# Kernel optimization log

Hardware: AMD Instinct MI355X
Metric: run time of the kernel (lower is better)

Reference implementation:

```python
import jax, jax.numpy as jnp
import numpy as np

# dims
T, B, D = 128, 512, 512          # seq, batch, d_input = dim_aug_state*n_agent
M, H, DH, DFF = 6, 2, 32, 64     # mem_len, heads, d_head_inner, d_ff_inner
ACT = 64                          # dim_action*n_agent
BG = 0.1                          # GRU-gate bias (GTrXL)


def _ln(t, g, b):
    mu = t.mean(-1, keepdims=True)
    var = ((t - mu) ** 2).mean(-1, keepdims=True)
    return (t - mu) / jnp.sqrt(var + 1e-5) * g + b


def _rel_shift(x):
    # x: [T, J, B, H] -> TransformerXL relative shift
    Tq, J = x.shape[0], x.shape[1]
    zp = jnp.zeros((Tq, 1) + x.shape[2:], x.dtype)
    x = jnp.concatenate([zp, x], axis=1)              # [T, J+1, B, H]
    x = x.reshape((J + 1, Tq) + x.shape[2:])[1:]      # [J, T, B, H]
    return x.reshape((Tq, J) + x.shape[2:])


def _gate(x, y, W, b):
    # GRU-style gating g(x, y): x = residual stream, y = new branch output
    lin = lambda t, i: t @ W[i] + b[i]
    r = jax.nn.sigmoid(lin(y, 0) + lin(x, 1))
    z = jax.nn.sigmoid(lin(y, 2) + lin(x, 3) - BG)
    h = jnp.tanh(lin(y, 4) + (r * x) @ W[5] + b[5])
    return (1.0 - z) * x + z * h


def setup_inputs() -> dict:
    key = jax.random.key(0)
    ks = iter(jax.random.split(key, 32))
    rn = lambda shape, s=0.02: jax.random.normal(next(ks), shape, jnp.float32) * s
    return dict(
        aug_states=jax.random.normal(next(ks), (T, B, D), jnp.float32),
        action=jax.random.normal(next(ks), (B, ACT), jnp.float32),
        memory=jnp.zeros((M, B, D), jnp.float32),
        W_q=rn((D, H * DH)), W_kv=rn((D, 2 * H * DH)), W_p=rn((D, H * DH)), W_out=rn((H * DH, D)),
        u=rn((H, DH)), v=rn((H, DH)),
        ln1_g=jnp.ones(D), ln1_b=jnp.zeros(D), ln2_g=jnp.ones(D), ln2_b=jnp.zeros(D),
        ff_W1=rn((D, DFF)), ff_b1=jnp.zeros(DFF), ff_W2=rn((DFF, D)), ff_b2=jnp.zeros(D),
        g1_W=rn((6, D, D)), g1_b=jnp.zeros((6, D)), g2_W=rn((6, D, D)), g2_b=jnp.zeros((6, D)),
        d1_W=rn((D, 1024)), d1_b=jnp.zeros(1024),
        d2_W=rn((1024 + ACT, 512)), d2_b=jnp.zeros(512),
        d3_W=rn((512, 300)), d3_b=jnp.zeros(300),
        d4_W=rn((300, 1)), d4_b=jnp.zeros(1),
    )


def reference(aug_states, action, memory, W_q, W_kv, W_p, W_out, u, v,
              ln1_g, ln1_b, ln2_g, ln2_b, ff_W1, ff_b1, ff_W2, ff_b2,
              g1_W, g1_b, g2_W, g2_b, d1_W, d1_b, d2_W, d2_b, d3_W, d3_b, d4_W, d4_b):
    x = aug_states                                    # [T, B, D]
    J = T + M
    # sinusoidal relative position embeddings for positions J-1 .. 0
    pos = jnp.arange(J - 1, -1, -1.0, dtype=jnp.float32)
    inv_freq = 1.0 / (10000.0 ** (jnp.arange(0, D, 2, dtype=jnp.float32) / D))
    si = pos[:, None] * inv_freq[None, :]
    pos_emb = jnp.concatenate([jnp.sin(si), jnp.cos(si)], axis=-1)   # [J, D]

    # --- stable (pre-LN + gated) TransformerXL layer ---
    src2 = _ln(x, ln1_g, ln1_b)
    cat = jnp.concatenate([memory, src2], axis=0)     # [J, B, D]
    k, vv = jnp.split(cat @ W_kv, 2, axis=-1)
    q = (src2 @ W_q).reshape(T, B, H, DH)
    k = k.reshape(J, B, H, DH)
    vv = vv.reshape(J, B, H, DH)
    p = (pos_emb @ W_p).reshape(J, H, DH)
    content = jnp.einsum("ibhd,jbhd->ijbh", q + u, k)
    position = _rel_shift(jnp.einsum("ibhd,jhd->ijbh", q + v, p))
    attn = content + position                         # [T, J, B, H]
    mask = jnp.arange(J)[None, :] > (jnp.arange(T)[:, None] + M)     # causal w/ memory offset
    attn = jnp.where(mask[:, :, None, None], -jnp.inf, attn)
    attn = jax.nn.softmax(attn * (1.0 / np.sqrt(DH)), axis=1)
    av = jnp.einsum("ijbh,jbhd->ibhd", attn, vv).reshape(T, B, H * DH)
    src = _gate(x, av @ W_out, g1_W, g1_b)
    ff = jax.nn.relu(_ln(src, ln2_g, ln2_b) @ ff_W1 + ff_b1) @ ff_W2 + ff_b2
    out = _gate(src, ff, g2_W, g2_b)                  # [T, B, D]

    # --- mean pool + MLP critic head ---
    ts = out.mean(axis=0)                             # [B, D]
    h1 = jax.nn.relu(ts @ d1_W + d1_b)
    h = jnp.concatenate([h1, action], axis=1)
    h = jax.nn.relu(h @ d2_W + d2_b)
    h = jax.nn.relu(h @ d3_W + d3_b)
    return jax.nn.relu(h @ d4_W + d4_b)               # [B, 1]
```

## Files before the change

kernel.cpp:

```cpp
#include <hip/hip_runtime.h>
#include <math.h>

namespace {

constexpr int kT = 128, kB = 512, kD = 512, kM = 6, kH = 2;
constexpr int kJ = kT + kM;
constexpr float kBG = 0.1f;
constexpr int kTB = kT * kB;
constexpr int kBK = 32;

typedef __attribute__((ext_vector_type(8))) short bf16x8;
typedef __attribute__((ext_vector_type(4))) float f32x4;
typedef __attribute__((ext_vector_type(8))) unsigned short us8;
typedef __attribute__((ext_vector_type(4))) unsigned short us4;

__device__ __forceinline__ float sigmoidf_(float x) {
  return 1.0f / (1.0f + __expf(-x));
}

__device__ __forceinline__ unsigned short bf16u(float f) {
  union { float f; unsigned u; } c; c.f = f;
  unsigned r = c.u + 0x7fffu + ((c.u >> 16) & 1u);
  return (unsigned short)(r >> 16);
}

__device__ __forceinline__ float b2f(unsigned short u) {
  union { unsigned u; float f; } c; c.u = (unsigned)u << 16;
  return c.f;
}

__device__ __forceinline__ void gl_lds16(const void* g, void* l) {
  __builtin_amdgcn_global_load_lds(
      (const __attribute__((address_space(1))) unsigned int*)g,
      (__attribute__((address_space(3))) unsigned int*)l, 16, 0, 0);
}

template <int N>
__device__ __forceinline__ void wvm_() {
  asm volatile("s_waitcnt vmcnt(%0)" :: "n"(N) : "memory");
}
__device__ __forceinline__ void bar_() { __builtin_amdgcn_s_barrier(); }
__device__ __forceinline__ void cfence_() { asm volatile("" ::: "memory"); }

__global__ __launch_bounds__(256) void transp_kernel(const float* __restrict__ W,
                                                     unsigned short* __restrict__ Wt,
                                                     int K, int N) {
  __shared__ float t[32][33];
  const int n0 = blockIdx.x * 32, k0 = blockIdx.y * 32;
  const float* Wb = W + (size_t)blockIdx.z * K * N;
  unsigned short* Wtb = Wt + (size_t)blockIdx.z * K * N;
  int tx = threadIdx.x & 31, ty = threadIdx.x >> 5;
#pragma unroll
  for (int r = 0; r < 32; r += 8)
    t[ty + r][tx] = Wb[(size_t)(k0 + ty + r) * N + n0 + tx];
  __syncthreads();
#pragma unroll
  for (int r = 0; r < 32; r += 8)
    Wtb[(size_t)(n0 + ty + r) * K + k0 + tx] = bf16u(t[tx][ty + r]);
}

__global__ __launch_bounds__(256) void conv_bf16_kernel(const float* __restrict__ in,
                                                        unsigned short* __restrict__ outb,
                                                        size_t n) {
  size_t idx = ((size_t)blockIdx.x * 256 + threadIdx.x) * 8;
  if (idx >= n) return;
  float4 a = *(const float4*)(in + idx);
  float4 c = *(const float4*)(in + idx + 4);
  us8 o;
  o[0] = bf16u(a.x); o[1] = bf16u(a.y); o[2] = bf16u(a.z); o[3] = bf16u(a.w);
  o[4] = bf16u(c.x); o[5] = bf16u(c.y); o[6] = bf16u(c.z); o[7] = bf16u(c.w);
  *(us8*)(outb + idx) = o;
}

__global__ __launch_bounds__(256) void ln1_dual_kernel(const float* __restrict__ in,
                                                       const float* __restrict__ g,
                                                       const float* __restrict__ b,
                                                       unsigned short* __restrict__ outLN,
                                                       unsigned short* __restrict__ outRaw,
                                                       int nrows) {
  int wave = threadIdx.x >> 6, lane = threadIdx.x & 63;
  int row = blockIdx.x * 4 + wave;
  if (row >= nrows) return;
  const float* p = in + (size_t)row * kD + lane * 8;
  float4 a = *(const float4*)p;
  float4 c = *(const float4*)(p + 4);
  float v[8] = {a.x, a.y, a.z, a.w, c.x, c.y, c.z, c.w};
  float s = 0.f;
#pragma unroll
  for (int i = 0; i < 8; ++i) s += v[i];
#pragma unroll
  for (int off = 32; off; off >>= 1) s += __shfl_xor(s, off);
  float mu = s * (1.0f / 512.0f);
  float q = 0.f;
#pragma unroll
  for (int i = 0; i < 8; ++i) { float d = v[i] - mu; q += d * d; }
#pragma unroll
  for (int off = 32; off; off >>= 1) q += __shfl_xor(q, off);
  float rstd = rsqrtf(q * (1.0f / 512.0f) + 1e-5f);
  us8 oln, oraw;
#pragma unroll
  for (int i = 0; i < 8; ++i) {
    int col = lane * 8 + i;
    oln[i] = bf16u((v[i] - mu) * rstd * g[col] + b[col]);
    oraw[i] = bf16u(v[i]);
  }
  size_t off8 = (size_t)row * kD + lane * 8;
  *(us8*)(outLN + off8) = oln;
  *(us8*)(outRaw + off8) = oraw;
}

__global__ __launch_bounds__(256) void ln_b16_kernel(const unsigned short* __restrict__ in,
                                                     const float* __restrict__ g,
                                                     const float* __restrict__ b,
                                                     unsigned short* __restrict__ outb,
                                                     int nrows) {
  int wave = threadIdx.x >> 6, lane = threadIdx.x & 63;
  int row = blockIdx.x * 4 + wave;
  if (row >= nrows) return;
  us8 iv = *(const us8*)(in + (size_t)row * kD + lane * 8);
  float v[8];
#pragma unroll
  for (int i = 0; i < 8; ++i) v[i] = b2f(iv[i]);
  float s = 0.f;
#pragma unroll
  for (int i = 0; i < 8; ++i) s += v[i];
#pragma unroll
  for (int off = 32; off; off >>= 1) s += __shfl_xor(s, off);
  float mu = s * (1.0f / 512.0f);
  float q = 0.f;
#pragma unroll
  for (int i = 0; i < 8; ++i) { float d = v[i] - mu; q += d * d; }
#pragma unroll
  for (int off = 32; off; off >>= 1) q += __shfl_xor(q, off);
  float rstd = rsqrtf(q * (1.0f / 512.0f) + 1e-5f);
  us8 o;
#pragma unroll
  for (int i = 0; i < 8; ++i) {
    int col = lane * 8 + i;
    o[i] = bf16u((v[i] - mu) * rstd * g[col] + b[col]);
  }
  *(us8*)(outb + (size_t)row * kD + lane * 8) = o;
}

template <int TN, int EPI>
__global__ __launch_bounds__(256) void mfma_gemm_bt(
    const unsigned short* __restrict__ A, const unsigned short* __restrict__ Bt,
    int K, const float* __restrict__ bias, void* __restrict__ Cv, int N) {
  constexpr int MI = (TN == 128) ? 4 : 2;
  constexpr int NJ = 4;
  constexpr int BCH = TN * 64 / 1024;
  constexpr int NLD = 2 + BCH / 4;
  __shared__ __align__(16) unsigned short As[3][128 * kBK];
  __shared__ __align__(16) unsigned short Bs[3][TN * kBK];
  const int tid = threadIdx.x;
  const int lane = tid & 63, wv = tid >> 6;
  const int ml = lane & 15, qd = lane >> 4;
  const int m0 = blockIdx.y * 128, n0 = blockIdx.x * TN;
  const int mw0 = (TN == 128) ? (wv >> 1) * 64 : wv * 32;
  const int nw0 = (TN == 128) ? (wv & 1) * 64 : 0;
  const size_t ldA = (size_t)K * 2, ldB = (size_t)K * 2;
  const char* Ab = (const char*)A + (size_t)m0 * ldA;
  const char* Bb = (const char*)Bt + (size_t)n0 * ldB;
  auto stg = [&](int k0, int buf) {
#pragma unroll
    for (int c = wv; c < 8; c += 4) {
      int fb = c * 1024 + lane * 16;
      gl_lds16(Ab + (size_t)(fb >> 6) * ldA + (fb & 63) + (size_t)k0 * 2,
               (char*)As[buf] + fb);
    }
#pragma unroll
    for (int c = wv; c < BCH; c += 4) {
      int fb = c * 1024 + lane * 16;
      gl_lds16(Bb + (size_t)(fb >> 6) * ldB + (fb & 63) + (size_t)k0 * 2,
               (char*)Bs[buf] + fb);
    }
  };
  f32x4 acc[MI][NJ];
#pragma unroll
  for (int i = 0; i < MI; ++i)
#pragma unroll
    for (int j = 0; j < NJ; ++j) acc[i][j] = (f32x4)0.f;
  stg(0, 0);
  stg(kBK, 1);
  int cb = 0;
  for (int k0 = 0; k0 < K; k0 += kBK) {
    const int sb = (cb == 0) ? 2 : cb - 1;
    if (k0 + 2 * kBK < K) { stg(k0 + 2 * kBK, sb); wvm_<2 * NLD>(); }
    else if (k0 + kBK < K) { wvm_<NLD>(); }
    else { wvm_<0>(); }
    bar_(); cfence_();
    bf16x8 af[MI], bfr[NJ];
#pragma unroll
    for (int i = 0; i < MI; ++i)
      af[i] = *(const bf16x8*)(As[cb] + (mw0 + i * 16 + ml) * kBK + qd * 8);
#pragma unroll
    for (int j = 0; j < NJ; ++j)
      bfr[j] = *(const bf16x8*)(Bs[cb] + (nw0 + j * 16 + ml) * kBK + qd * 8);
    __builtin_amdgcn_s_setprio(1);
#pragma unroll
    for (int i = 0; i < MI; ++i)
#pragma unroll
      for (int j = 0; j < NJ; ++j)
        acc[i][j] = __builtin_amdgcn_mfma_f32_16x16x32_bf16(af[i], bfr[j], acc[i][j], 0, 0, 0);
    __builtin_amdgcn_s_setprio(0);
    cfence_(); bar_();
    cb = (cb == 2) ? 0 : cb + 1;
  }
#pragma unroll
  for (int i = 0; i < MI; ++i)
#pragma unroll
    for (int j = 0; j < NJ; ++j)
#pragma unroll
      for (int r = 0; r < 4; ++r) {
        int m = m0 + mw0 + i * 16 + qd * 4 + r;
        int n = n0 + nw0 + j * 16 + ml;
        float val = acc[i][j][r];
        if (EPI >= 2) val += bias[n];
        if (EPI == 2) val = fmaxf(val, 0.f);
        size_t idx = (size_t)m * N + n;
        if (EPI == 0) ((float*)Cv)[idx] = val;
        else ((unsigned short*)Cv)[idx] = bf16u(val);
      }
}

template <int NBLOG>
__device__ __forceinline__ void xcd_decode(int& m0, int& n0, int tileN) {
  const int L = blockIdx.x;
  const int xcd = L & 7;
  const int s = L >> 3;
  const int mgPerX = (int)(gridDim.x >> (3 + NBLOG));
  const int mg = xcd * mgPerX + (s >> NBLOG);
  const int nb = s & ((1 << NBLOG) - 1);
  m0 = mg * 128;
  n0 = nb * tileN;
}

__global__ __launch_bounds__(256) void mfma_gate_rz(
    const unsigned short* __restrict__ Yb, const unsigned short* __restrict__ Xb,
    const unsigned short* __restrict__ Wt, const float* __restrict__ gb,
    unsigned short* __restrict__ RX, unsigned short* __restrict__ Zq) {
  __shared__ __align__(16) unsigned short As[3][128 * kBK];
  __shared__ __align__(16) unsigned short Bs[3][128 * kBK];
  const int tid = threadIdx.x;
  const int lane = tid & 63, wv = tid >> 6;
  const int ml = lane & 15, qd = lane >> 4;
  int m0, n0;
  xcd_decode<3>(m0, n0, 128);
  const int nhalf = n0 >> 9;
  const int n0e = n0 & 511;
  const int mw0 = (wv >> 1) * 64, nw0 = (wv & 1) * 64;
  const size_t ld = (size_t)kD * 2;
  const size_t DD = (size_t)kD * kD;
  const char* Abp[2]; const char* Bbp[2];
  {
    const unsigned short* Ap[2] = {Yb, Xb};
#pragma unroll
    for (int p = 0; p < 2; ++p) {
      Abp[p] = (const char*)Ap[p] + (size_t)m0 * ld;
      Bbp[p] = (const char*)(Wt + (size_t)(2 * nhalf + p) * DD) + (size_t)n0e * ld;
    }
  }
  auto stg = [&](const char* Ab, const char* Bb, int k0, int buf) {
#pragma unroll
    for (int c = wv; c < 8; c += 4) {
      int fb = c * 1024 + lane * 16;
      size_t go = (size_t)(fb >> 6) * ld + (fb & 63) + (size_t)k0 * 2;
      gl_lds16(Ab + go, (char*)As[buf] + fb);
      gl_lds16(Bb + go, (char*)Bs[buf] + fb);
    }
  };
  f32x4 acc[4][4];
#pragma unroll
  for (int i = 0; i < 4; ++i)
#pragma unroll
    for (int j = 0; j < 4; ++j) acc[i][j] = (f32x4)0.f;
  stg(Abp[0], Bbp[0], 0, 0);
  stg(Abp[0], Bbp[0], kBK, 1);
  int cb = 0;
#pragma unroll
  for (int p = 0; p < 2; ++p) {
    for (int k = 0; k < 16; ++k) {
      const int sb = (cb == 0) ? 2 : cb - 1;
      if (k < 14) { stg(Abp[p], Bbp[p], (k + 2) * kBK, sb); wvm_<8>(); }
      else if (p < 1) { stg(Abp[p + 1], Bbp[p + 1], (k - 14) * kBK, sb); wvm_<8>(); }
      else if (k == 14) { wvm_<4>(); }
      else { wvm_<0>(); }
      bar_(); cfence_();
      bf16x8 af[4], bfr[4];
#pragma unroll
      for (int i = 0; i < 4; ++i)
        af[i] = *(const bf16x8*)(As[cb] + (mw0 + i * 16 + ml) * kBK + qd * 8);
#pragma unroll
      for (int j = 0; j < 4; ++j)
        bfr[j] = *(const bf16x8*)(Bs[cb] + (nw0 + j * 16 + ml) * kBK + qd * 8);
      __builtin_amdgcn_s_setprio(1);
#pragma unroll
      for (int i = 0; i < 4; ++i)
#pragma unroll
        for (int j = 0; j < 4; ++j)
          acc[i][j] = __builtin_amdgcn_mfma_f32_16x16x32_bf16(af[i], bfr[j], acc[i][j], 0, 0, 0);
      __builtin_amdgcn_s_setprio(0);
      cfence_(); bar_();
      cb = (cb == 2) ? 0 : cb + 1;
    }
  }
  if (nhalf == 0) {
#pragma unroll
    for (int i = 0; i < 4; ++i)
#pragma unroll
      for (int j = 0; j < 4; ++j)
#pragma unroll
        for (int r = 0; r < 4; ++r) {
          int m = m0 + mw0 + i * 16 + qd * 4 + r;
          int n = n0e + nw0 + j * 16 + ml;
          float rg = sigmoidf_(acc[i][j][r] + gb[n] + gb[kD + n]);
          size_t idx = (size_t)m * kD + n;
          RX[idx] = bf16u(rg * b2f(Xb[idx]));
        }
  } else {
#pragma unroll
    for (int i = 0; i < 4; ++i)
#pragma unroll
      for (int j = 0; j < 4; ++j)
#pragma unroll
        for (int r = 0; r < 4; ++r) {
          int m = m0 + mw0 + i * 16 + qd * 4 + r;
          int n = n0e + nw0 + j * 16 + ml;
          float z = sigmoidf_(acc[i][j][r] + gb[2 * kD + n] + gb[3 * kD + n] - kBG);
          Zq[(size_t)m * kD + n] = (unsigned short)(z * 65535.f + 0.5f);
        }
  }
}

template <bool POOL>
__global__ __launch_bounds__(256) void mfma_gate_h(
    const unsigned short* __restrict__ Yb, const unsigned short* __restrict__ RXb,
    const unsigned short* __restrict__ Xb, const unsigned short* __restrict__ Wt,
    const float* __restrict__ gb, const unsigned short* __restrict__ Zq,
    unsigned short* __restrict__ OUTb, float* __restrict__ TS, int rowoff) {
  __shared__ __align__(16) unsigned short As[3][128 * kBK];
  __shared__ __align__(16) unsigned short Bs[3][128 * kBK];
  const int tid = threadIdx.x;
  const int lane = tid & 63, wv = tid >> 6;
  const int ml = lane & 15, qd = lane >> 4;
  int m0, n0;
  xcd_decode<2>(m0, n0, 128);
  const int mw0 = (wv >> 1) * 64, nw0 = (wv & 1) * 64;
  const size_t ld = (size_t)kD * 2;
  const size_t DD = (size_t)kD * kD;
  const char* Abp[2]; const char* Bbp[2];
  {
    const unsigned short* Ap[2] = {Yb, RXb};
#pragma unroll
    for (int p = 0; p < 2; ++p) {
      Abp[p] = (const char*)Ap[p] + (size_t)m0 * ld;
      Bbp[p] = (const char*)(Wt + (size_t)(4 + p) * DD) + (size_t)n0 * ld;
    }
  }
  auto stg = [&](const char* Ab, const char* Bb, int k0, int buf) {
#pragma unroll
    for (int c = wv; c < 8; c += 4) {
      int fb = c * 1024 + lane * 16;
      size_t go = (size_t)(fb >> 6) * ld + (fb & 63) + (size_t)k0 * 2;
      gl_lds16(Ab + go, (char*)As[buf] + fb);
      gl_lds16(Bb + go, (char*)Bs[buf] + fb);
    }
  };
  f32x4 acc[4][4];
#pragma unroll
  for (int i = 0; i < 4; ++i)
#pragma unroll
    for (int j = 0; j < 4; ++j) acc[i][j] = (f32x4)0.f;
  stg(Abp[0], Bbp[0], 0, 0);
  stg(Abp[0], Bbp[0], kBK, 1);
  int cb = 0;
#pragma unroll
  for (int p = 0; p < 2; ++p) {
    for (int k = 0; k < 16; ++k) {
      const int sb = (cb == 0) ? 2 : cb - 1;
      if (k < 14) { stg(Abp[p], Bbp[p], (k + 2) * kBK, sb); wvm_<8>(); }
      else if (p < 1) { stg(Abp[p + 1], Bbp[p + 1], (k - 14) * kBK, sb); wvm_<8>(); }
      else if (k == 14) { wvm_<4>(); }
      else { wvm_<0>(); }
      bar_(); cfence_();
      bf16x8 af[4], bfr[4];
#pragma unroll
      for (int i = 0; i < 4; ++i)
        af[i] = *(const bf16x8*)(As[cb] + (mw0 + i * 16 + ml) * kBK + qd * 8);
#pragma unroll
      for (int j = 0; j < 4; ++j)
        bfr[j] = *(const bf16x8*)(Bs[cb] + (nw0 + j * 16 + ml) * kBK + qd * 8);
      __builtin_amdgcn_s_setprio(1);
#pragma unroll
      for (int i = 0; i < 4; ++i)
#pragma unroll
        for (int j = 0; j < 4; ++j)
          acc[i][j] = __builtin_amdgcn_mfma_f32_16x16x32_bf16(af[i], bfr[j], acc[i][j], 0, 0, 0);
      __builtin_amdgcn_s_setprio(0);
      cfence_(); bar_();
      cb = (cb == 2) ? 0 : cb + 1;
    }
  }
#pragma unroll
  for (int i = 0; i < 4; ++i)
#pragma unroll
    for (int j = 0; j < 4; ++j)
#pragma unroll
      for (int r = 0; r < 4; ++r) {
        int m = m0 + mw0 + i * 16 + qd * 4 + r;
        int n = n0 + nw0 + j * 16 + ml;
        size_t idx = (size_t)m * kD + n;
        float z = (float)Zq[idx] * (1.0f / 65535.0f);
        float hc = tanhf(acc[i][j][r] + gb[4 * kD + n] + gb[5 * kD + n]);
        float val = (1.0f - z) * b2f(Xb[idx]) + z * hc;
        if (POOL) {
          int b = (rowoff + m) & (kB - 1);
          atomicAdd(TS + (size_t)b * kD + n, val * (1.0f / kT));
        } else {
          OUTb[idx] = bf16u(val);
        }
      }
}

__global__ __launch_bounds__(64) void posp_kernel(const float* __restrict__ Wp,
                                                  float* __restrict__ P) {
  __shared__ float emb[512];
  int jj = blockIdx.x;
  int t = threadIdx.x;
  float pos = (float)(kJ - 1 - jj);
#pragma unroll
  for (int r = 0; r < 8; ++r) {
    int d = t + r * 64;
    int i = (d < 256) ? d : d - 256;
    float invf = expf(-((float)(2 * i) * (1.0f / 512.0f)) * 9.210340371976184f);
    float si = pos * invf;
    emb[d] = (d < 256) ? sinf(si) : cosf(si);
  }
  __syncthreads();
  float acc = 0.f;
  for (int d = 0; d < 512; ++d) acc = fmaf(emb[d], Wp[d * 64 + t], acc);
  P[jj * 64 + t] = acc;
}

__global__ __launch_bounds__(128) void attn_kernel(
    const float* __restrict__ Q, const unsigned short* __restrict__ KV,
    const float* __restrict__ P, const float* __restrict__ U,
    const float* __restrict__ V, unsigned short* __restrict__ AV) {
  __shared__ float ks[kJ][32];
  __shared__ float vs[kJ][32];
  __shared__ float ps[32][kJ + 2];
  const int b = blockIdx.x, h = blockIdx.y;
  const int tid = threadIdx.x;
  for (int idx = tid; idx < kJ * 8; idx += 128) {
    int j = idx >> 3, seg = idx & 7;
    const unsigned short* src = KV + ((size_t)(j * kB + b)) * 128 + h * 32 + seg * 4;
    us4 kq = *(const us4*)src;
    us4 vq = *(const us4*)(src + 64);
#pragma unroll
    for (int e = 0; e < 4; ++e) {
      ks[j][seg * 4 + e] = b2f(kq[e]);
      vs[j][seg * 4 + e] = b2f(vq[e]);
    }
  }
  for (int idx = tid; idx < kJ * 8; idx += 128) {
    int j = idx >> 3, seg = idx & 7;
    float4 pq = *(const float4*)(P + j * 64 + h * 32 + seg * 4);
    ps[seg * 4 + 0][j] = pq.x;
    ps[seg * 4 + 1][j] = pq.y;
    ps[seg * 4 + 2][j] = pq.z;
    ps[seg * 4 + 3][j] = pq.w;
  }
  __syncthreads();
  const int i = tid;
  float qu[32], qv[32];
  const float* qp = Q + ((size_t)(i * kB + b)) * 64 + h * 32;
#pragma unroll
  for (int d = 0; d < 32; ++d) {
    float qd = qp[d];
    qu[d] = qd + U[h * 32 + d];
    qv[d] = qd + V[h * 32 + d];
  }
  float m = -INFINITY, l = 0.f, acc[32] = {};
  const float scale = 0.17677669529663687f;
  for (int j = 0; j <= i + kM; ++j) {
    float s = 0.f;
#pragma unroll
    for (int d = 0; d < 32; d += 4) {
      float4 k4 = *(const float4*)&ks[j][d];
      s = fmaf(qu[d + 0], k4.x, s);
      s = fmaf(qu[d + 1], k4.y, s);
      s = fmaf(qu[d + 2], k4.z, s);
      s = fmaf(qu[d + 3], k4.w, s);
    }
    int jj = j + (kT - 1) - i;
#pragma unroll
    for (int d = 0; d < 32; ++d) s = fmaf(qv[d], ps[d][jj], s);
    float ls = s * scale;
    float nm = fmaxf(m, ls);
    float w = __expf(ls - nm);
    float f = __expf(m - nm);
    l = l * f + w;
#pragma unroll
    for (int d = 0; d < 32; d += 4) {
      float4 v4 = *(const float4*)&vs[j][d];
      acc[d + 0] = fmaf(acc[d + 0], f, w * v4.x);
      acc[d + 1] = fmaf(acc[d + 1], f, w * v4.y);
      acc[d + 2] = fmaf(acc[d + 2], f, w * v4.z);
      acc[d + 3] = fmaf(acc[d + 3], f, w * v4.w);
    }
    m = nm;
  }
  float inv = 1.0f / l;
  unsigned short* o = AV + ((size_t)(i * kB + b)) * 64 + h * 32;
#pragma unroll
  for (int d = 0; d < 32; ++d) o[d] = bf16u(acc[d] * inv);
}

template <int ACTF, bool DUAL>
__global__ __launch_bounds__(256) void gemm_kernel(
    const float* __restrict__ A1, const float* __restrict__ Bm1, int K1,
    const float* __restrict__ A2, const float* __restrict__ Bm2, int K2,
    const float* __restrict__ bias, float* __restrict__ C, int Mrows, int N) {
  __shared__ float As[16][68];
  __shared__ float Bs[16][68];
  const int tid = threadIdx.x;
  const int tx = tid & 15, ty = tid >> 4;
  const int m0 = blockIdx.y * 64, n0 = blockIdx.x * 64;
  const int ar = tid >> 2, aseg = tid & 3;
  float acc[4][4] = {};
#pragma unroll
  for (int pass = 0; pass < (DUAL ? 2 : 1); ++pass) {
    const float* A = (DUAL && pass) ? A2 : A1;
    const float* Bm = (DUAL && pass) ? Bm2 : Bm1;
    const int K = (DUAL && pass) ? K2 : K1;
    for (int k0 = 0; k0 < K; k0 += 16) {
      {
        int row = m0 + ar;
        int kb = k0 + aseg * 4;
        float x0 = 0.f, x1 = 0.f, x2 = 0.f, x3 = 0.f;
        if (row < Mrows) {
          const float* ap = A + (size_t)row * K + kb;
          if (kb + 3 < K) {
            float4 t = *(const float4*)ap;
            x0 = t.x; x1 = t.y; x2 = t.z; x3 = t.w;
          } else {
            if (kb + 0 < K) x0 = ap[0];
            if (kb + 1 < K) x1 = ap[1];
            if (kb + 2 < K) x2 = ap[2];
          }
        }
        As[aseg * 4 + 0][ar] = x0;
        As[aseg * 4 + 1][ar] = x1;
        As[aseg * 4 + 2][ar] = x2;
        As[aseg * 4 + 3][ar] = x3;
      }
      {
        int krow = k0 + ty;
        int nb = n0 + tx * 4;
        float y0 = 0.f, y1 = 0.f, y2 = 0.f, y3 = 0.f;
        if (krow < K) {
          const float* bp = Bm + (size_t)krow * N + nb;
          if (nb + 3 < N) {
            float4 t = *(const float4*)bp;
            y0 = t.x; y1 = t.y; y2 = t.z; y3 = t.w;
          } else {
            if (nb + 0 < N) y0 = bp[0];
            if (nb + 1 < N) y1 = bp[1];
            if (nb + 2 < N) y2 = bp[2];
          }
        }
        *(float4*)&Bs[ty][tx * 4] = make_float4(y0, y1, y2, y3);
      }
      __syncthreads();
#pragma unroll
      for (int kk = 0; kk < 16; ++kk) {
        float a[4], bb[4];
        *(float4*)a = *(const float4*)&As[kk][ty * 4];
        *(float4*)bb = *(const float4*)&Bs[kk][tx * 4];
#pragma unroll
        for (int i = 0; i < 4; ++i)
#pragma unroll
          for (int j = 0; j < 4; ++j) acc[i][j] = fmaf(a[i], bb[j], acc[i][j]);
      }
      __syncthreads();
    }
  }
#pragma unroll
  for (int i = 0; i < 4; ++i) {
    int m = m0 + ty * 4 + i;
    if (m >= Mrows) continue;
#pragma unroll
    for (int j = 0; j < 4; ++j) {
      int n = n0 + tx * 4 + j;
      if (n >= N) continue;
      float val = acc[i][j];
      if (bias) val += bias[n];
      if (ACTF == 1) val = fmaxf(val, 0.f);
      C[(size_t)m * N + n] = val;
    }
  }
}

}

extern "C" void kernel_launch(void* const* d_in, const int* in_sizes, int n_in,
                              void* d_out, int out_size, void* d_ws, size_t ws_size,
                              hipStream_t stream) {
  (void)in_sizes; (void)n_in; (void)out_size;
  const float* aug    = (const float*)d_in[0];
  const float* action = (const float*)d_in[1];
  const float* memory = (const float*)d_in[2];
  const float* W_q    = (const float*)d_in[3];
  const float* W_kv   = (const float*)d_in[4];
  const float* W_p    = (const float*)d_in[5];
  const float* W_out  = (const float*)d_in[6];
  const float* u      = (const float*)d_in[7];
  const float* v      = (const float*)d_in[8];
  const float* ln1_g  = (const float*)d_in[9];
  const float* ln1_b  = (const float*)d_in[10];
  const float* ln2_g  = (const float*)d_in[11];
  const float* ln2_b  = (const float*)d_in[12];
  const float* ff_W1  = (const float*)d_in[13];
  const float* ff_b1  = (const float*)d_in[14];
  const float* ff_W2  = (const float*)d_in[15];
  const float* ff_b2  = (const float*)d_in[16];
  const float* g1_W   = (const float*)d_in[17];
  const float* g1_b   = (const float*)d_in[18];
  const float* g2_W   = (const float*)d_in[19];
  const float* g2_b   = (const float*)d_in[20];
  const float* d1_W   = (const float*)d_in[21];
  const float* d1_b   = (const float*)d_in[22];
  const float* d2_W   = (const float*)d_in[23];
  const float* d2_b   = (const float*)d_in[24];
  const float* d3_W   = (const float*)d_in[25];
  const float* d3_b   = (const float*)d_in[26];
  const float* d4_W   = (const float*)d_in[27];
  const float* d4_b   = (const float*)d_in[28];
  float* out = (float*)d_out;

  char* base = (char*)d_ws;
  auto alloc = [&](size_t bytes) -> char* {
    char* p = base;
    base += (bytes + 255) & ~(size_t)255;
    return p;
  };
  unsigned short* Wqt  = (unsigned short*)alloc((size_t)64 * 512 * 2);
  unsigned short* Wkvt = (unsigned short*)alloc((size_t)128 * 512 * 2);
  unsigned short* Wot  = (unsigned short*)alloc((size_t)512 * 64 * 2);
  unsigned short* Wf1t = (unsigned short*)alloc((size_t)64 * 512 * 2);
  unsigned short* Wf2t = (unsigned short*)alloc((size_t)512 * 64 * 2);
  unsigned short* G1t  = (unsigned short*)alloc((size_t)6 * 512 * 512 * 2);
  unsigned short* G2t  = (unsigned short*)alloc((size_t)6 * 512 * 512 * 2);
  unsigned short* Memb = (unsigned short*)alloc((size_t)3072 * 512 * 2);
  unsigned short* KVb  = (unsigned short*)alloc((size_t)kJ * kB * 128 * 2);
  float* Qb  = (float*)alloc((size_t)kTB * 64 * 4);
  unsigned short* AVb = (unsigned short*)alloc((size_t)kTB * 64 * 2);
  unsigned short* Xb  = (unsigned short*)alloc((size_t)kTB * kD * 2);
  float* Pb  = (float*)alloc((size_t)kJ * 64 * 4);
  float* TSb = (float*)alloc((size_t)kB * kD * 4);
  float* H1b = (float*)alloc((size_t)kB * 1024 * 4);
  float* H2b = (float*)alloc((size_t)kB * 512 * 4);
  float* H3b = (float*)alloc((size_t)kB * 320 * 4);
  size_t fixedBytes = (size_t)(base - (char*)d_ws);
  const size_t ln1Bytes = (size_t)kTB * kD * 2;
  int nch = 1;
  while (nch < 32) {
    size_t chunkBytes = (size_t)(kTB / nch) * 4224 + 4096;
    size_t reuse = chunkBytes > ln1Bytes ? chunkBytes : ln1Bytes;
    if (fixedBytes + reuse <= ws_size) break;
    nch <<= 1;
  }
  const int CR = kTB / nch;
  char* R = base;
  unsigned short* L1b = (unsigned short*)R;
  char* rp = R;
  auto ralloc = [&](size_t bytes) -> char* {
    char* p = rp;
    rp += (bytes + 255) & ~(size_t)255;
    return p;
  };
  unsigned short* Ycb   = (unsigned short*)ralloc((size_t)CR * 512 * 2);
  unsigned short* RXcb  = (unsigned short*)ralloc((size_t)CR * 512 * 2);
  unsigned short* SRCcb = (unsigned short*)ralloc((size_t)CR * 512 * 2);
  unsigned short* LN2cb = (unsigned short*)ralloc((size_t)CR * 512 * 2);
  unsigned short* F1cb  = (unsigned short*)ralloc((size_t)CR * 64 * 2);
  unsigned short* Zqb = LN2cb;

  const float* np = nullptr;
  const int MG = CR / 128;

  hipMemsetAsync(TSb, 0, (size_t)kB * kD * sizeof(float), stream);
  transp_kernel<<<dim3(2, 16, 1), 256, 0, stream>>>(W_q, Wqt, 512, 64);
  transp_kernel<<<dim3(4, 16, 1), 256, 0, stream>>>(W_kv, Wkvt, 512, 128);
  transp_kernel<<<dim3(16, 2, 1), 256, 0, stream>>>(W_out, Wot, 64, 512);
  transp_kernel<<<dim3(2, 16, 1), 256, 0, stream>>>(ff_W1, Wf1t, 512, 64);
  transp_kernel<<<dim3(16, 2, 1), 256, 0, stream>>>(ff_W2, Wf2t, 64, 512);
  transp_kernel<<<dim3(16, 16, 6), 256, 0, stream>>>(g1_W, G1t, 512, 512);
  transp_kernel<<<dim3(16, 16, 6), 256, 0, stream>>>(g2_W, G2t, 512, 512);
  conv_bf16_kernel<<<(3072 * 512 / 8 + 255) / 256, 256, 0, stream>>>(
      memory, Memb, (size_t)3072 * 512);
  ln1_dual_kernel<<<kTB / 4, 256, 0, stream>>>(aug, ln1_g, ln1_b, L1b, Xb, kTB);
  mfma_gemm_bt<128, 1><<<dim3(1, 3072 / 128), 256, 0, stream>>>(
      Memb, Wkvt, 512, np, KVb, 128);
  mfma_gemm_bt<128, 1><<<dim3(1, kTB / 128), 256, 0, stream>>>(
      L1b, Wkvt, 512, np, KVb + (size_t)3072 * 128, 128);
  mfma_gemm_bt<64, 0><<<dim3(1, kTB / 128), 256, 0, stream>>>(
      L1b, Wqt, 512, np, Qb, 64);
  posp_kernel<<<kJ, 64, 0, stream>>>(W_p, Pb);
  attn_kernel<<<dim3(kB, kH), 128, 0, stream>>>(Qb, KVb, Pb, u, v, AVb);

  for (int c = 0; c < nch; ++c) {
    const int R0 = c * CR;
    const unsigned short* Xc = Xb + (size_t)R0 * kD;
    mfma_gemm_bt<128, 1><<<dim3(4, MG), 256, 0, stream>>>(
        AVb + (size_t)R0 * 64, Wot, 64, np, Ycb, 512);
    mfma_gate_rz<<<8 * MG, 256, 0, stream>>>(Ycb, Xc, G1t, g1_b, RXcb, Zqb);
    mfma_gate_h<false><<<4 * MG, 256, 0, stream>>>(
        Ycb, RXcb, Xc, G1t, g1_b, Zqb, SRCcb, nullptr, R0);
    ln_b16_kernel<<<CR / 4, 256, 0, stream>>>(SRCcb, ln2_g, ln2_b, LN2cb, CR);
    mfma_gemm_bt<64, 2><<<dim3(1, MG), 256, 0, stream>>>(
        LN2cb, Wf1t, 512, ff_b1, F1cb, 64);
    mfma_gemm_bt<128, 3><<<dim3(4, MG), 256, 0, stream>>>(
        F1cb, Wf2t, 64, ff_b2, Ycb, 512);
    mfma_gate_rz<<<8 * MG, 256, 0, stream>>>(Ycb, SRCcb, G2t, g2_b, RXcb, Zqb);
    mfma_gate_h<true><<<4 * MG, 256, 0, stream>>>(
        Ycb, RXcb, SRCcb, G2t, g2_b, Zqb, nullptr, TSb, R0);
  }

  gemm_kernel<1, false><<<dim3(16, kB / 64), 256, 0, stream>>>(
      TSb, d1_W, 512, np, np, 0, d1_b, H1b, kB, 1024);
  gemm_kernel<1, true><<<dim3(8, kB / 64), 256, 0, stream>>>(
      H1b, d2_W, 1024, action, d2_W + (size_t)1024 * 512, 64, d2_b, H2b, kB, 512);
  gemm_kernel<1, false><<<dim3(5, kB / 64), 256, 0, stream>>>(
      H2b, d3_W, 512, np, np, 0, d3_b, H3b, kB, 300);
  gemm_kernel<1, false><<<dim3(1, kB / 64), 256, 0, stream>>>(
      H3b, d4_W, 300, np, np, 0, d4_b, out, kB, 1);
}
```

Baseline: 1.547 ms.

## Drop persistent bf16 residual buffer, reconvert per chunk, chunk LN1 projections

The full-size bf16 copy of the input (Xb) is no longer written by the LN1 kernel. Each main-loop chunk now reconverts its slice of the fp32 input into a reused buffer, and gate_h writes its output in place over that buffer. The LN1/Q/KV projection is split into chunks over a smaller scratch area, and the main chunk count starts at 2 to fit the reduced workspace. The setprio hints around the MFMA loop are also removed. This saves a large global write and shrinks the working set for better cache locality, at the cost of re-reading the fp32 input and launching more kernels.

```diff
diff --git a/kernel.cpp b/kernel.cpp
--- a/kernel.cpp
+++ b/kernel.cpp
@@ -106,7 +106,7 @@
   }
   size_t off8 = (size_t)row * kD + lane * 8;
   *(us8*)(outLN + off8) = oln;
-  *(us8*)(outRaw + off8) = oraw;
+  if (outRaw) *(us8*)(outRaw + off8) = oraw;
 }
 
 __global__ __launch_bounds__(256) void ln_b16_kernel(const unsigned short* __restrict__ in,
@@ -196,13 +196,11 @@
 #pragma unroll
     for (int j = 0; j < NJ; ++j)
       bfr[j] = *(const bf16x8*)(Bs[cb] + (nw0 + j * 16 + ml) * kBK + qd * 8);
-    __builtin_amdgcn_s_setprio(1);
 #pragma unroll
     for (int i = 0; i < MI; ++i)
 #pragma unroll
       for (int j = 0; j < NJ; ++j)
         acc[i][j] = __builtin_amdgcn_mfma_f32_16x16x32_bf16(af[i], bfr[j], acc[i][j], 0, 0, 0);
-    __builtin_amdgcn_s_setprio(0);
     cfence_(); bar_();
     cb = (cb == 2) ? 0 : cb + 1;
   }
@@ -638,10 +636,12 @@
   const float* d4_b   = (const float*)d_in[28];
   float* out = (float*)d_out;
 
+  auto A256 = [](size_t b) { return (b + 255) & ~(size_t)255; };
+
   char* base = (char*)d_ws;
   auto alloc = [&](size_t bytes) -> char* {
     char* p = base;
-    base += (bytes + 255) & ~(size_t)255;
+    base += A256(bytes);
     return p;
   };
   unsigned short* Wqt  = (unsigned short*)alloc((size_t)64 * 512 * 2);
@@ -651,43 +651,48 @@
   unsigned short* Wf2t = (unsigned short*)alloc((size_t)512 * 64 * 2);
   unsigned short* G1t  = (unsigned short*)alloc((size_t)6 * 512 * 512 * 2);
   unsigned short* G2t  = (unsigned short*)alloc((size_t)6 * 512 * 512 * 2);
-  unsigned short* Memb = (unsigned short*)alloc((size_t)3072 * 512 * 2);
-  unsigned short* KVb  = (unsigned short*)alloc((size_t)kJ * kB * 128 * 2);
-  float* Qb  = (float*)alloc((size_t)kTB * 64 * 4);
-  unsigned short* AVb = (unsigned short*)alloc((size_t)kTB * 64 * 2);
-  unsigned short* Xb  = (unsigned short*)alloc((size_t)kTB * kD * 2);
+  unsigned short* AVb  = (unsigned short*)alloc((size_t)kTB * 64 * 2);
   float* Pb  = (float*)alloc((size_t)kJ * 64 * 4);
   float* TSb = (float*)alloc((size_t)kB * kD * 4);
   float* H1b = (float*)alloc((size_t)kB * 1024 * 4);
   float* H2b = (float*)alloc((size_t)kB * 512 * 4);
   float* H3b = (float*)alloc((size_t)kB * 320 * 4);
-  size_t fixedBytes = (size_t)(base - (char*)d_ws);
-  const size_t ln1Bytes = (size_t)kTB * kD * 2;
-  int nch = 1;
-  while (nch < 32) {
-    size_t chunkBytes = (size_t)(kTB / nch) * 4224 + 4096;
-    size_t reuse = chunkBytes > ln1Bytes ? chunkBytes : ln1Bytes;
-    if (fixedBytes + reuse <= ws_size) break;
+  const size_t persist = (size_t)(base - (char*)d_ws);
+
+  const size_t membB = A256((size_t)3072 * 512 * 2);
+  const size_t kvbB  = A256((size_t)kJ * kB * 128 * 2);
+  const size_t qbB   = A256((size_t)kTB * 64 * 4);
+  int nchp = 1;
+  while (nchp < 32) {
+    size_t l1B = A256((size_t)(kTB / nchp) * 512 * 2);
+    if (persist + membB + kvbB + qbB + l1B <= ws_size) break;
+    nchp <<= 1;
+  }
+  int nch = 2;
+  while (nch < 64) {
+    size_t CRi = (size_t)kTB / nch;
+    size_t mainB = 4 * A256(CRi * 512 * 2) + A256(CRi * 64 * 2);
+    if (persist + mainB <= ws_size) break;
     nch <<= 1;
   }
-  const int CR = kTB / nch;
-  char* R = base;
-  unsigned short* L1b = (unsigned short*)R;
-  char* rp = R;
-  auto ralloc = [&](size_t bytes) -> char* {
-    char* p = rp;
-    rp += (bytes + 255) & ~(size_t)255;
-    return p;
-  };
-  unsigned short* Ycb   = (unsigned short*)ralloc((size_t)CR * 512 * 2);
-  unsigned short* RXcb  = (unsigned short*)ralloc((size_t)CR * 512 * 2);
-  unsigned short* SRCcb = (unsigned short*)ralloc((size_t)CR * 512 * 2);
-  unsigned short* LN2cb = (unsigned short*)ralloc((size_t)CR * 512 * 2);
-  unsigned short* F1cb  = (unsigned short*)ralloc((size_t)CR * 64 * 2);
+  const int CRp = kTB / nchp;
+  const int CR  = kTB / nch;
+  const int MG  = CR / 128;
+
+  char* U = base;
+  unsigned short* Memb = (unsigned short*)U;
+  unsigned short* KVb  = (unsigned short*)(U + membB);
+  float*          Qb   = (float*)(U + membB + kvbB);
+  unsigned short* L1c  = (unsigned short*)(U + membB + kvbB + qbB);
+  const size_t rb = A256((size_t)CR * 512 * 2);
+  unsigned short* XSc   = (unsigned short*)U;
+  unsigned short* Ycb   = (unsigned short*)(U + rb);
+  unsigned short* RXcb  = (unsigned short*)(U + 2 * rb);
+  unsigned short* LN2cb = (unsigned short*)(U + 3 * rb);
+  unsigned short* F1cb  = (unsigned short*)(U + 4 * rb);
   unsigned short* Zqb = LN2cb;
 
   const float* np = nullptr;
-  const int MG = CR / 128;
 
   hipMemsetAsync(TSb, 0, (size_t)kB * kD * sizeof(float), stream);
   transp_kernel<<<dim3(2, 16, 1), 256, 0, stream>>>(W_q, Wqt, 512, 64);
@@ -697,34 +702,39 @@
   transp_kernel<<<dim3(16, 2, 1), 256, 0, stream>>>(ff_W2, Wf2t, 64, 512);
   transp_kernel<<<dim3(16, 16, 6), 256, 0, stream>>>(g1_W, G1t, 512, 512);
   transp_kernel<<<dim3(16, 16, 6), 256, 0, stream>>>(g2_W, G2t, 512, 512);
+  posp_kernel<<<kJ, 64, 0, stream>>>(W_p, Pb);
   conv_bf16_kernel<<<(3072 * 512 / 8 + 255) / 256, 256, 0, stream>>>(
       memory, Memb, (size_t)3072 * 512);
-  ln1_dual_kernel<<<kTB / 4, 256, 0, stream>>>(aug, ln1_g, ln1_b, L1b, Xb, kTB);
   mfma_gemm_bt<128, 1><<<dim3(1, 3072 / 128), 256, 0, stream>>>(
       Memb, Wkvt, 512, np, KVb, 128);
-  mfma_gemm_bt<128, 1><<<dim3(1, kTB / 128), 256, 0, stream>>>(
-      L1b, Wkvt, 512, np, KVb + (size_t)3072 * 128, 128);
-  mfma_gemm_bt<64, 0><<<dim3(1, kTB / 128), 256, 0, stream>>>(
-      L1b, Wqt, 512, np, Qb, 64);
-  posp_kernel<<<kJ, 64, 0, stream>>>(W_p, Pb);
+  for (int pc = 0; pc < nchp; ++pc) {
+    const int R0 = pc * CRp;
+    ln1_dual_kernel<<<CRp / 4, 256, 0, stream>>>(
+        aug + (size_t)R0 * kD, ln1_g, ln1_b, L1c, nullptr, CRp);
+    mfma_gemm_bt<128, 1><<<dim3(1, CRp / 128), 256, 0, stream>>>(
+        L1c, Wkvt, 512, np, KVb + (size_t)(3072 + R0) * 128, 128);
+    mfma_gemm_bt<64, 0><<<dim3(1, CRp / 128), 256, 0, stream>>>(
+        L1c, Wqt, 512, np, Qb + (size_t)R0 * 64, 64);
+  }
   attn_kernel<<<dim3(kB, kH), 128, 0, stream>>>(Qb, KVb, Pb, u, v, AVb);
 
   for (int c = 0; c < nch; ++c) {
     const int R0 = c * CR;
-    const unsigned short* Xc = Xb + (size_t)R0 * kD;
+    conv_bf16_kernel<<<(int)(((size_t)CR * 512 / 8 + 255) / 256), 256, 0, stream>>>(
+        aug + (size_t)R0 * kD, XSc, (size_t)CR * 512);
     mfma_gemm_bt<128, 1><<<dim3(4, MG), 256, 0, stream>>>(
         AVb + (size_t)R0 * 64, Wot, 64, np, Ycb, 512);
-    mfma_gate_rz<<<8 * MG, 256, 0, stream>>>(Ycb, Xc, G1t, g1_b, RXcb, Zqb);
+    mfma_gate_rz<<<8 * MG, 256, 0, stream>>>(Ycb, XSc, G1t, g1_b, RXcb, Zqb);
     mfma_gate_h<false><<<4 * MG, 256, 0, stream>>>(
-        Ycb, RXcb, Xc, G1t, g1_b, Zqb, SRCcb, nullptr, R0);
-    ln_b16_kernel<<<CR / 4, 256, 0, stream>>>(SRCcb, ln2_g, ln2_b, LN2cb, CR);
+        Ycb, RXcb, XSc, G1t, g1_b, Zqb, XSc, nullptr, R0);
+    ln_b16_kernel<<<CR / 4, 256, 0, stream>>>(XSc, ln2_g, ln2_b, LN2cb, CR);
     mfma_gemm_bt<64, 2><<<dim3(1, MG), 256, 0, stream>>>(
         LN2cb, Wf1t, 512, ff_b1, F1cb, 64);
     mfma_gemm_bt<128, 3><<<dim3(4, MG), 256, 0, stream>>>(
         F1cb, Wf2t, 64, ff_b2, Ycb, 512);
-    mfma_gate_rz<<<8 * MG, 256, 0, stream>>>(Ycb, SRCcb, G2t, g2_b, RXcb, Zqb);
+    mfma_gate_rz<<<8 * MG, 256, 0, stream>>>(Ycb, XSc, G2t, g2_b, RXcb, Zqb);
     mfma_gate_h<true><<<4 * MG, 256, 0, stream>>>(
-        Ycb, RXcb, SRCcb, G2t, g2_b, Zqb, nullptr, TSb, R0);
+        Ycb, RXcb, XSc, G2t, g2_b, Zqb, nullptr, TSb, R0);
   }
 
   gemm_kernel<1, false><<<dim3(16, kB / 64), 256, 0, stream>>>(
```

New measurement: 1.719 ms. 1.11x slower.
